# Performance work log

Hardware: AMD Instinct MI355X
Metric: run time of the kernel (lower is better)

## Reference

```python
import jax, jax.numpy as jnp
import numpy as np

VOCAB = 50000
E = 32            # embed_size; node state is E x E
LABELS = 10
DEPTH = 11        # perfect binary tree: 2^DEPTH - 1 = 2047 nodes, 1024 leaves
N_NODES = 2 ** DEPTH - 1
LN_EPS = 1e-5


def setup_inputs() -> dict:
    key = jax.random.key(0)
    ks = jax.random.split(key, 8)
    word_ids = jax.random.randint(ks[0], (N_NODES,), 0, VOCAB, dtype=jnp.int32)
    label = 3
    emb_table = jax.random.normal(ks[1], (VOCAB, E * E), dtype=jnp.float32) * 0.02
    Ww = jax.random.normal(ks[2], (E, E), dtype=jnp.float32) * (1.0 / np.sqrt(E))
    Wb = jax.random.normal(ks[3], (E,), dtype=jnp.float32) * 0.01
    gamma = jnp.ones((E, E), dtype=jnp.float32)   # LayerNorm((1,E,E)) affine weight
    beta = jnp.zeros((E, E), dtype=jnp.float32)
    Pw = jax.random.normal(ks[4], (LABELS, E * E), dtype=jnp.float32) * (1.0 / E)
    Pb = jnp.zeros((LABELS,), dtype=jnp.float32)
    return {"word_ids": word_ids, "label": label, "emb_table": emb_table,
            "Ww": Ww, "Wb": Wb, "gamma": gamma, "beta": beta, "Pw": Pw, "Pb": Pb}


def reference(word_ids, label, emb_table, Ww, Wb, gamma, beta, Pw, Pb):
    # word_ids: level-order ids of a perfect binary tree, children of within-level
    # index j at level d are indices 2j, 2j+1 at level d+1.
    embs = emb_table[word_ids].reshape(N_NODES, E, E)  # [N, E, E]

    def ln_relu(x):
        # torch LayerNorm((1,E,E)): normalize over the whole E*E matrix, affine per element
        mu = jnp.mean(x, axis=(1, 2), keepdims=True)
        var = jnp.var(x, axis=(1, 2), keepdims=True)
        y = (x - mu) * jax.lax.rsqrt(var + LN_EPS) * gamma + beta
        return jax.nn.relu(y)

    # leaves: level DEPTH-1
    start = 2 ** (DEPTH - 1) - 1
    h = ln_relu(embs[start:])  # [2^(DEPTH-1), E, E]
    # internal levels bottom-up; loop over fixed DEPTH-1 levels (not data dims)
    for d in range(DEPTH - 2, -1, -1):
        s = 2 ** d - 1
        cur = embs[s:s + 2 ** d]                     # [n_d, E, E]
        l, r = h[0::2], h[1::2]                      # children pairs
        x = jnp.einsum('nij,njk,nkl->nil', l, r, cur)
        x = x @ Ww.T + Wb                            # Linear applied row-wise
        h = ln_relu(x)

    root = h[0].reshape(-1)                          # [E*E]
    logits = root @ Pw.T + Pb                        # [LABELS]
    prediction = jnp.argmax(logits)
    loss = -jax.nn.log_softmax(logits)[label]
    return (prediction, loss)
```

## Files before the change

### kernel.cpp

```cpp
#include <hip/hip_runtime.h>
#include <hip/hip_bf16.h>

#define LN_EPS 1e-5f
#define TSB 40
#define TILEB (32 * TSB)

typedef __attribute__((ext_vector_type(8))) short bf16x8;
typedef __attribute__((ext_vector_type(16))) float f32x16;

__device__ __forceinline__ short bf16b(float f) {
  return __builtin_bit_cast(short, __float2bfloat16(f));
}

__device__ __forceinline__ void wave_reduce2(float& s1, float& s2) {
  #pragma unroll
  for (int off = 32; off; off >>= 1) {
    s1 += __shfl_xor(s1, off);
    s2 += __shfl_xor(s2, off);
  }
}

__device__ __forceinline__ bf16x8 frag_ld(const short* t, int l, int k0) {
  return *(const bf16x8*)&t[(l & 31) * TSB + ((l >> 5) << 3) + k0];
}

__device__ __forceinline__ int cd_row(int r, int l) {
  return (r & 3) + 8 * (r >> 2) + 4 * (l >> 5);
}

__device__ __forceinline__ void cd_store(short* t, int l, const f32x16 d,
                                         bool transp) {
  const int col = l & 31;
  if (transp) {
    #pragma unroll
    for (int r = 0; r < 16; ++r) t[col * TSB + cd_row(r, l)] = bf16b(d[r]);
  } else {
    #pragma unroll
    for (int r = 0; r < 16; ++r) t[cd_row(r, l) * TSB + col] = bf16b(d[r]);
  }
}

struct NodeParams {
  bf16x8 w0, w1;
  float wb;
  float ga[16], be[16];
};

__device__ __forceinline__ NodeParams load_params(const float* __restrict__ Ww,
    const float* __restrict__ Wb, const float* __restrict__ gamma,
    const float* __restrict__ beta, int l) {
  NodeParams P;
  const int n = l & 31, kh = (l >> 5) * 8;
  float w[8];
  *(float4*)&w[0] = *(const float4*)&Ww[n * 32 + kh];
  *(float4*)&w[4] = *(const float4*)&Ww[n * 32 + kh + 4];
  #pragma unroll
  for (int i = 0; i < 8; ++i) P.w0[i] = bf16b(w[i]);
  *(float4*)&w[0] = *(const float4*)&Ww[n * 32 + kh + 16];
  *(float4*)&w[4] = *(const float4*)&Ww[n * 32 + kh + 20];
  #pragma unroll
  for (int i = 0; i < 8; ++i) P.w1[i] = bf16b(w[i]);
  P.wb = Wb[n];
  #pragma unroll
  for (int r = 0; r < 16; ++r) {
    const int idx = cd_row(r, l) * 32 + n;
    P.ga[r] = gamma[idx];
    P.be[r] = beta[idx];
  }
  return P;
}

__device__ __forceinline__ f32x16 mm32(const short* A, const short* B, int l) {
  f32x16 acc = {};
  acc = __builtin_amdgcn_mfma_f32_32x32x16_bf16(frag_ld(A, l, 0),
                                                frag_ld(B, l, 0), acc, 0, 0, 0);
  acc = __builtin_amdgcn_mfma_f32_32x32x16_bf16(frag_ld(A, l, 16),
                                                frag_ld(B, l, 16), acc, 0, 0, 0);
  return acc;
}

__device__ __forceinline__ void node_mfma(short* A, short* Bt, const short* Ct,
                                          const NodeParams& P, int l,
                                          short* dst, bool transpOut,
                                          float* fout) {
  f32x16 t1 = mm32(A, Bt, l);
  cd_store(A, l, t1, false);
  f32x16 t2 = mm32(A, Ct, l);
  cd_store(Bt, l, t2, false);
  f32x16 x = {};
  x = __builtin_amdgcn_mfma_f32_32x32x16_bf16(frag_ld(Bt, l, 0), P.w0, x, 0, 0, 0);
  x = __builtin_amdgcn_mfma_f32_32x32x16_bf16(frag_ld(Bt, l, 16), P.w1, x, 0, 0, 0);
  float s1 = 0.f, s2 = 0.f;
  #pragma unroll
  for (int r = 0; r < 16; ++r) {
    x[r] += P.wb;
    s1 += x[r];
    s2 += x[r] * x[r];
  }
  wave_reduce2(s1, s2);
  const float mu = s1 * (1.f / 1024.f);
  const float rs = rsqrtf(s2 * (1.f / 1024.f) - mu * mu + LN_EPS);
  #pragma unroll
  for (int r = 0; r < 16; ++r)
    x[r] = fmaxf((x[r] - mu) * rs * P.ga[r] + P.be[r], 0.f);
  if (fout) {
    #pragma unroll
    for (int r = 0; r < 16; ++r) fout[cd_row(r, l) * 32 + (l & 31)] = x[r];
  } else {
    cd_store(dst, l, x, transpOut);
  }
}

__device__ __forceinline__ void stage_f32(short* dst,
                                          const float* __restrict__ src, int l,
                                          bool transp) {
  float v[16];
  #pragma unroll
  for (int q = 0; q < 4; ++q)
    *(float4*)&v[q * 4] = *(const float4*)&src[l * 16 + q * 4];
  const int row = l >> 1, c0 = (l & 1) * 16;
  if (transp) {
    #pragma unroll
    for (int i = 0; i < 16; ++i) dst[(c0 + i) * TSB + row] = bf16b(v[i]);
  } else {
    #pragma unroll
    for (int i = 0; i < 8; ++i) {
      unsigned lo = (unsigned short)bf16b(v[2 * i]);
      unsigned hi = (unsigned short)bf16b(v[2 * i + 1]);
      ((unsigned*)dst)[row * (TSB / 2) + (c0 >> 1) + i] = lo | (hi << 16);
    }
  }
}

__device__ __forceinline__ void stage_bf16(short* dst,
                                           const short* __restrict__ src, int l,
                                           bool transp) {
  short v[16];
  *(bf16x8*)&v[0] = *(const bf16x8*)&src[l * 16];
  *(bf16x8*)&v[8] = *(const bf16x8*)&src[l * 16 + 8];
  const int row = l >> 1, c0 = (l & 1) * 16;
  if (transp) {
    #pragma unroll
    for (int i = 0; i < 16; ++i) dst[(c0 + i) * TSB + row] = v[i];
  } else {
    #pragma unroll
    for (int i = 0; i < 8; ++i) {
      unsigned lo = (unsigned short)v[2 * i];
      unsigned hi = (unsigned short)v[2 * i + 1];
      ((unsigned*)dst)[row * (TSB / 2) + (c0 >> 1) + i] = lo | (hi << 16);
    }
  }
}

__device__ __forceinline__ void copy_out(short* __restrict__ dst, const short* t,
                                         int u) {
  if (u < 128) {
    const int row = u >> 2, c0 = (u & 3) * 8;
    *(bf16x8*)&dst[row * 32 + c0] = *(const bf16x8*)&t[row * TSB + c0];
  }
}

__device__ __forceinline__ void leaf_ln(short* dst, const float* __restrict__ src,
                                        const float* __restrict__ gamma,
                                        const float* __restrict__ beta, int l,
                                        bool transp) {
  float v[16], ga[16], be[16];
  #pragma unroll
  for (int q = 0; q < 4; ++q) {
    *(float4*)&v[q * 4] = *(const float4*)&src[l * 16 + q * 4];
    *(float4*)&ga[q * 4] = *(const float4*)&gamma[l * 16 + q * 4];
    *(float4*)&be[q * 4] = *(const float4*)&beta[l * 16 + q * 4];
  }
  float s1 = 0.f, s2 = 0.f;
  #pragma unroll
  for (int i = 0; i < 16; ++i) { s1 += v[i]; s2 += v[i] * v[i]; }
  wave_reduce2(s1, s2);
  const float mu = s1 * (1.f / 1024.f);
  const float rs = rsqrtf(s2 * (1.f / 1024.f) - mu * mu + LN_EPS);
  #pragma unroll
  for (int i = 0; i < 16; ++i)
    v[i] = fmaxf((v[i] - mu) * rs * ga[i] + be[i], 0.f);
  const int row = l >> 1, c0 = (l & 1) * 16;
  if (transp) {
    #pragma unroll
    for (int i = 0; i < 16; ++i) dst[(c0 + i) * TSB + row] = bf16b(v[i]);
  } else {
    #pragma unroll
    for (int i = 0; i < 8; ++i) {
      unsigned lo = (unsigned short)bf16b(v[2 * i]);
      unsigned hi = (unsigned short)bf16b(v[2 * i + 1]);
      ((unsigned*)dst)[row * (TSB / 2) + (c0 >> 1) + i] = lo | (hi << 16);
    }
  }
}

__global__ __launch_bounds__(256) void k_bot(
    const int* __restrict__ wid, const float* __restrict__ emb,
    const float* __restrict__ Ww, const float* __restrict__ Wb,
    const float* __restrict__ gamma, const float* __restrict__ beta,
    short* __restrict__ h8) {
  __shared__ __align__(16) short pool[7 * TILEB];
  const int u = threadIdx.x, blk = blockIdx.x;
  const int wv = u >> 6, l = u & 63;
  NodeParams P = load_params(Ww, Wb, gamma, beta, l);
  if (wv == 0)
    stage_f32(pool + 4 * TILEB, emb + (size_t)wid[511 + 2 * blk] * 1024, l, true);
  else if (wv == 1)
    stage_f32(pool + 5 * TILEB, emb + (size_t)wid[512 + 2 * blk] * 1024, l, true);
  else if (wv == 2)
    stage_f32(pool + 6 * TILEB, emb + (size_t)wid[255 + blk] * 1024, l, true);
  leaf_ln(pool + wv * TILEB, emb + (size_t)wid[1023 + 4 * blk + wv] * 1024,
          gamma, beta, l, (wv & 1) != 0);
  __syncthreads();
  if (wv < 2)
    node_mfma(pool + 2 * wv * TILEB, pool + (2 * wv + 1) * TILEB,
              pool + (4 + wv) * TILEB, P, l, pool + (4 + wv) * TILEB, wv == 1,
              nullptr);
  __syncthreads();
  if (wv == 0)
    node_mfma(pool + 4 * TILEB, pool + 5 * TILEB, pool + 6 * TILEB, P, l,
              pool + 6 * TILEB, false, nullptr);
  __syncthreads();
  copy_out(h8 + (size_t)blk * 1024, pool + 6 * TILEB, u);
}

__global__ __launch_bounds__(256) void k_mid(
    const int* __restrict__ wid, const float* __restrict__ emb,
    const float* __restrict__ Ww, const float* __restrict__ Wb,
    const float* __restrict__ gamma, const float* __restrict__ beta,
    const short* __restrict__ hin, short* __restrict__ hout,
    int cb, int pb, int gb) {
  __shared__ __align__(16) short pool[15 * TILEB];
  const int u = threadIdx.x, blk = blockIdx.x;
  const int wv = u >> 6, l = u & 63;
  NodeParams P = load_params(Ww, Wb, gamma, beta, l);
  stage_bf16(pool + 2 * wv * TILEB, hin + (size_t)(8 * blk + 2 * wv) * 1024, l,
             false);
  stage_bf16(pool + (2 * wv + 1) * TILEB,
             hin + (size_t)(8 * blk + 2 * wv + 1) * 1024, l, true);
  stage_f32(pool + (8 + wv) * TILEB,
            emb + (size_t)wid[cb + 4 * blk + wv] * 1024, l, true);
  if (wv < 2)
    stage_f32(pool + (12 + wv) * TILEB,
              emb + (size_t)wid[pb + 2 * blk + wv] * 1024, l, true);
  else if (wv == 2)
    stage_f32(pool + 14 * TILEB, emb + (size_t)wid[gb + blk] * 1024, l, true);
  __syncthreads();
  node_mfma(pool + 2 * wv * TILEB, pool + (2 * wv + 1) * TILEB,
            pool + (8 + wv) * TILEB, P, l, pool + (8 + wv) * TILEB,
            (wv & 1) != 0, nullptr);
  __syncthreads();
  if (wv < 2)
    node_mfma(pool + (8 + 2 * wv) * TILEB, pool + (9 + 2 * wv) * TILEB,
              pool + (12 + wv) * TILEB, P, l, pool + (12 + wv) * TILEB,
              wv == 1, nullptr);
  __syncthreads();
  if (wv == 0)
    node_mfma(pool + 12 * TILEB, pool + 13 * TILEB, pool + 14 * TILEB, P, l,
              pool + 14 * TILEB, false, nullptr);
  __syncthreads();
  copy_out(hout + (size_t)blk * 1024, pool + 14 * TILEB, u);
}

__global__ __launch_bounds__(256) void k_top(
    const int* __restrict__ wid, const float* __restrict__ emb,
    const float* __restrict__ Ww, const float* __restrict__ Wb,
    const float* __restrict__ gamma, const float* __restrict__ beta,
    const float* __restrict__ Pw, const float* __restrict__ Pb,
    const int* __restrict__ label, const short* __restrict__ hin,
    float* __restrict__ out) {
  __shared__ __align__(16) short pool[7 * TILEB];
  __shared__ float rootf[1024];
  __shared__ float lred[10];
  const int u = threadIdx.x;
  const int wv = u >> 6, l = u & 63;
  NodeParams P = load_params(Ww, Wb, gamma, beta, l);
  stage_bf16(pool + wv * TILEB, hin + (size_t)wv * 1024, l, (wv & 1) != 0);
  if (wv == 0) stage_f32(pool + 4 * TILEB, emb + (size_t)wid[1] * 1024, l, true);
  else if (wv == 1) stage_f32(pool + 5 * TILEB, emb + (size_t)wid[2] * 1024, l, true);
  else if (wv == 2) stage_f32(pool + 6 * TILEB, emb + (size_t)wid[0] * 1024, l, true);
  __syncthreads();
  if (wv < 2)
    node_mfma(pool + 2 * wv * TILEB, pool + (2 * wv + 1) * TILEB,
              pool + (4 + wv) * TILEB, P, l, pool + (4 + wv) * TILEB, wv == 1,
              nullptr);
  __syncthreads();
  if (wv == 0)
    node_mfma(pool + 4 * TILEB, pool + 5 * TILEB, pool + 6 * TILEB, P, l,
              nullptr, false, rootf);
  __syncthreads();
  #pragma unroll
  for (int q = 0; q < 3; ++q) {
    const int c = wv + 4 * q;
    if (c < 10) {
      float p = 0.f;
      #pragma unroll
      for (int t = 0; t < 4; ++t) {
        float4 r4 = *(const float4*)&rootf[l * 16 + t * 4];
        float4 w4 = *(const float4*)&Pw[c * 1024 + l * 16 + t * 4];
        p += r4.x * w4.x + r4.y * w4.y + r4.z * w4.z + r4.w * w4.w;
      }
      #pragma unroll
      for (int off = 32; off; off >>= 1) p += __shfl_xor(p, off);
      if (l == 0) lred[c] = p + Pb[c];
    }
  }
  __syncthreads();
  if (u == 0) {
    float mmax = lred[0];
    int am = 0;
    #pragma unroll
    for (int c = 1; c < 10; ++c)
      if (lred[c] > mmax) { mmax = lred[c]; am = c; }
    float sum = 0.f;
    #pragma unroll
    for (int c = 0; c < 10; ++c) sum += expf(lred[c] - mmax);
    const float loss = -(lred[label[0]] - mmax - logf(sum));
    out[0] = (float)am;
    out[1] = loss;
  }
}

extern "C" void kernel_launch(void* const* d_in, const int* in_sizes, int n_in,
                              void* d_out, int out_size, void* d_ws, size_t ws_size,
                              hipStream_t stream) {
  const int* wid = (const int*)d_in[0];
  const int* label = (const int*)d_in[1];
  const float* emb = (const float*)d_in[2];
  const float* Ww = (const float*)d_in[3];
  const float* Wb = (const float*)d_in[4];
  const float* g = (const float*)d_in[5];
  const float* b = (const float*)d_in[6];
  const float* Pw = (const float*)d_in[7];
  const float* Pb = (const float*)d_in[8];
  float* out = (float*)d_out;

  short* h8 = (short*)d_ws;
  short* h5 = h8 + 256 * 1024;
  short* h2 = h5 + 32 * 1024;

  k_bot<<<256, 256, 0, stream>>>(wid, emb, Ww, Wb, g, b, h8);
  k_mid<<<32, 256, 0, stream>>>(wid, emb, Ww, Wb, g, b, h8, h5, 127, 63, 31);
  k_mid<<<4, 256, 0, stream>>>(wid, emb, Ww, Wb, g, b, h5, h2, 15, 7, 3);
  k_top<<<1, 256, 0, stream>>>(wid, emb, Ww, Wb, g, b, Pw, Pb, label, h2, out);
}
```

Before: 30.82 us.

## Regroup tree levels into three 512-thread launches instead of four

```diff
diff --git a/kernel.cpp b/kernel.cpp
--- a/kernel.cpp
+++ b/kernel.cpp
@@ -194,104 +194,126 @@
   }
 }
 
-__global__ __launch_bounds__(256) void k_bot(
+__global__ __launch_bounds__(512) void k_bot7(
     const int* __restrict__ wid, const float* __restrict__ emb,
     const float* __restrict__ Ww, const float* __restrict__ Wb,
     const float* __restrict__ gamma, const float* __restrict__ beta,
-    short* __restrict__ h8) {
-  __shared__ __align__(16) short pool[7 * TILEB];
-  const int u = threadIdx.x, blk = blockIdx.x;
-  const int wv = u >> 6, l = u & 63;
-  NodeParams P = load_params(Ww, Wb, gamma, beta, l);
-  if (wv == 0)
-    stage_f32(pool + 4 * TILEB, emb + (size_t)wid[511 + 2 * blk] * 1024, l, true);
-  else if (wv == 1)
-    stage_f32(pool + 5 * TILEB, emb + (size_t)wid[512 + 2 * blk] * 1024, l, true);
-  else if (wv == 2)
-    stage_f32(pool + 6 * TILEB, emb + (size_t)wid[255 + blk] * 1024, l, true);
-  leaf_ln(pool + wv * TILEB, emb + (size_t)wid[1023 + 4 * blk + wv] * 1024,
-          gamma, beta, l, (wv & 1) != 0);
-  __syncthreads();
-  if (wv < 2)
-    node_mfma(pool + 2 * wv * TILEB, pool + (2 * wv + 1) * TILEB,
-              pool + (4 + wv) * TILEB, P, l, pool + (4 + wv) * TILEB, wv == 1,
-              nullptr);
-  __syncthreads();
-  if (wv == 0)
-    node_mfma(pool + 4 * TILEB, pool + 5 * TILEB, pool + 6 * TILEB, P, l,
-              pool + 6 * TILEB, false, nullptr);
-  __syncthreads();
-  copy_out(h8 + (size_t)blk * 1024, pool + 6 * TILEB, u);
-}
-
-__global__ __launch_bounds__(256) void k_mid(
-    const int* __restrict__ wid, const float* __restrict__ emb,
-    const float* __restrict__ Ww, const float* __restrict__ Wb,
-    const float* __restrict__ gamma, const float* __restrict__ beta,
-    const short* __restrict__ hin, short* __restrict__ hout,
-    int cb, int pb, int gb) {
+    short* __restrict__ h7) {
   __shared__ __align__(16) short pool[15 * TILEB];
   const int u = threadIdx.x, blk = blockIdx.x;
   const int wv = u >> 6, l = u & 63;
   NodeParams P = load_params(Ww, Wb, gamma, beta, l);
-  stage_bf16(pool + 2 * wv * TILEB, hin + (size_t)(8 * blk + 2 * wv) * 1024, l,
-             false);
-  stage_bf16(pool + (2 * wv + 1) * TILEB,
-             hin + (size_t)(8 * blk + 2 * wv + 1) * 1024, l, true);
-  stage_f32(pool + (8 + wv) * TILEB,
-            emb + (size_t)wid[cb + 4 * blk + wv] * 1024, l, true);
-  if (wv < 2)
-    stage_f32(pool + (12 + wv) * TILEB,
-              emb + (size_t)wid[pb + 2 * blk + wv] * 1024, l, true);
-  else if (wv == 2)
-    stage_f32(pool + 14 * TILEB, emb + (size_t)wid[gb + blk] * 1024, l, true);
-  __syncthreads();
-  node_mfma(pool + 2 * wv * TILEB, pool + (2 * wv + 1) * TILEB,
-            pool + (8 + wv) * TILEB, P, l, pool + (8 + wv) * TILEB,
-            (wv & 1) != 0, nullptr);
+  if (wv < 4)
+    stage_f32(pool + (8 + wv) * TILEB,
+              emb + (size_t)wid[511 + 4 * blk + wv] * 1024, l, true);
+  else if (wv < 6)
+    stage_f32(pool + (8 + wv) * TILEB,
+              emb + (size_t)wid[255 + 2 * blk + (wv - 4)] * 1024, l, true);
+  else if (wv == 6)
+    stage_f32(pool + 14 * TILEB, emb + (size_t)wid[127 + blk] * 1024, l, true);
+  leaf_ln(pool + wv * TILEB, emb + (size_t)wid[1023 + 8 * blk + wv] * 1024,
+          gamma, beta, l, (wv & 1) != 0);
+  __syncthreads();
+  if (wv < 4)
+    node_mfma(pool + 2 * wv * TILEB, pool + (2 * wv + 1) * TILEB,
+              pool + (8 + wv) * TILEB, P, l, pool + (8 + wv) * TILEB,
+              (wv & 1) != 0, nullptr);
   __syncthreads();
   if (wv < 2)
     node_mfma(pool + (8 + 2 * wv) * TILEB, pool + (9 + 2 * wv) * TILEB,
               pool + (12 + wv) * TILEB, P, l, pool + (12 + wv) * TILEB,
-              wv == 1, nullptr);
+              (wv & 1) != 0, nullptr);
   __syncthreads();
   if (wv == 0)
     node_mfma(pool + 12 * TILEB, pool + 13 * TILEB, pool + 14 * TILEB, P, l,
               pool + 14 * TILEB, false, nullptr);
   __syncthreads();
+  copy_out(h7 + (size_t)blk * 1024, pool + 14 * TILEB, u);
+}
+
+__global__ __launch_bounds__(512) void k_mid16(
+    const int* __restrict__ wid, const float* __restrict__ emb,
+    const float* __restrict__ Ww, const float* __restrict__ Wb,
+    const float* __restrict__ gamma, const float* __restrict__ beta,
+    const short* __restrict__ hin, short* __restrict__ hout) {
+  __shared__ __align__(16) short pool[15 * TILEB];
+  const int u = threadIdx.x, blk = blockIdx.x;
+  const int wv = u >> 6, l = u & 63;
+  NodeParams P = load_params(Ww, Wb, gamma, beta, l);
+  stage_bf16(pool + wv * TILEB, hin + (size_t)(8 * blk + wv) * 1024, l,
+             (wv & 1) != 0);
+  if (wv < 4)
+    stage_f32(pool + (8 + wv) * TILEB,
+              emb + (size_t)wid[63 + 4 * blk + wv] * 1024, l, true);
+  else if (wv < 6)
+    stage_f32(pool + (8 + wv) * TILEB,
+              emb + (size_t)wid[31 + 2 * blk + (wv - 4)] * 1024, l, true);
+  else if (wv == 6)
+    stage_f32(pool + 14 * TILEB, emb + (size_t)wid[15 + blk] * 1024, l, true);
+  __syncthreads();
+  if (wv < 4)
+    node_mfma(pool + 2 * wv * TILEB, pool + (2 * wv + 1) * TILEB,
+              pool + (8 + wv) * TILEB, P, l, pool + (8 + wv) * TILEB,
+              (wv & 1) != 0, nullptr);
+  __syncthreads();
+  if (wv < 2)
+    node_mfma(pool + (8 + 2 * wv) * TILEB, pool + (9 + 2 * wv) * TILEB,
+              pool + (12 + wv) * TILEB, P, l, pool + (12 + wv) * TILEB,
+              (wv & 1) != 0, nullptr);
+  __syncthreads();
+  if (wv == 0)
+    node_mfma(pool + 12 * TILEB, pool + 13 * TILEB, pool + 14 * TILEB, P, l,
+              pool + 14 * TILEB, false, nullptr);
+  __syncthreads();
   copy_out(hout + (size_t)blk * 1024, pool + 14 * TILEB, u);
 }
 
-__global__ __launch_bounds__(256) void k_top(
+__global__ __launch_bounds__(512) void k_top2(
     const int* __restrict__ wid, const float* __restrict__ emb,
     const float* __restrict__ Ww, const float* __restrict__ Wb,
     const float* __restrict__ gamma, const float* __restrict__ beta,
     const float* __restrict__ Pw, const float* __restrict__ Pb,
     const int* __restrict__ label, const short* __restrict__ hin,
     float* __restrict__ out) {
-  __shared__ __align__(16) short pool[7 * TILEB];
+  __shared__ __align__(16) short pool[31 * TILEB];
   __shared__ float rootf[1024];
   __shared__ float lred[10];
   const int u = threadIdx.x;
   const int wv = u >> 6, l = u & 63;
   NodeParams P = load_params(Ww, Wb, gamma, beta, l);
-  stage_bf16(pool + wv * TILEB, hin + (size_t)wv * 1024, l, (wv & 1) != 0);
-  if (wv == 0) stage_f32(pool + 4 * TILEB, emb + (size_t)wid[1] * 1024, l, true);
-  else if (wv == 1) stage_f32(pool + 5 * TILEB, emb + (size_t)wid[2] * 1024, l, true);
-  else if (wv == 2) stage_f32(pool + 6 * TILEB, emb + (size_t)wid[0] * 1024, l, true);
+  stage_bf16(pool + 2 * wv * TILEB, hin + (size_t)(2 * wv) * 1024, l, false);
+  stage_bf16(pool + (2 * wv + 1) * TILEB, hin + (size_t)(2 * wv + 1) * 1024, l,
+             true);
+  stage_f32(pool + (16 + wv) * TILEB, emb + (size_t)wid[7 + wv] * 1024, l, true);
+  if (wv < 4)
+    stage_f32(pool + (24 + wv) * TILEB, emb + (size_t)wid[3 + wv] * 1024, l, true);
+  else if (wv < 6)
+    stage_f32(pool + (24 + wv) * TILEB,
+              emb + (size_t)wid[1 + (wv - 4)] * 1024, l, true);
+  else if (wv == 6)
+    stage_f32(pool + 30 * TILEB, emb + (size_t)wid[0] * 1024, l, true);
+  __syncthreads();
+  node_mfma(pool + 2 * wv * TILEB, pool + (2 * wv + 1) * TILEB,
+            pool + (16 + wv) * TILEB, P, l, pool + (16 + wv) * TILEB,
+            (wv & 1) != 0, nullptr);
+  __syncthreads();
+  if (wv < 4)
+    node_mfma(pool + (16 + 2 * wv) * TILEB, pool + (17 + 2 * wv) * TILEB,
+              pool + (24 + wv) * TILEB, P, l, pool + (24 + wv) * TILEB,
+              (wv & 1) != 0, nullptr);
   __syncthreads();
   if (wv < 2)
-    node_mfma(pool + 2 * wv * TILEB, pool + (2 * wv + 1) * TILEB,
-              pool + (4 + wv) * TILEB, P, l, pool + (4 + wv) * TILEB, wv == 1,
-              nullptr);
+    node_mfma(pool + (24 + 2 * wv) * TILEB, pool + (25 + 2 * wv) * TILEB,
+              pool + (28 + wv) * TILEB, P, l, pool + (28 + wv) * TILEB,
+              (wv & 1) != 0, nullptr);
   __syncthreads();
   if (wv == 0)
-    node_mfma(pool + 4 * TILEB, pool + 5 * TILEB, pool + 6 * TILEB, P, l,
+    node_mfma(pool + 28 * TILEB, pool + 29 * TILEB, pool + 30 * TILEB, P, l,
               nullptr, false, rootf);
   __syncthreads();
   #pragma unroll
-  for (int q = 0; q < 3; ++q) {
-    const int c = wv + 4 * q;
+  for (int q = 0; q < 2; ++q) {
+    const int c = wv + 8 * q;
     if (c < 10) {
       float p = 0.f;
       #pragma unroll
@@ -335,12 +357,10 @@
   const float* Pb = (const float*)d_in[8];
   float* out = (float*)d_out;
 
-  short* h8 = (short*)d_ws;
-  short* h5 = h8 + 256 * 1024;
-  short* h2 = h5 + 32 * 1024;
-
-  k_bot<<<256, 256, 0, stream>>>(wid, emb, Ww, Wb, g, b, h8);
-  k_mid<<<32, 256, 0, stream>>>(wid, emb, Ww, Wb, g, b, h8, h5, 127, 63, 31);
-  k_mid<<<4, 256, 0, stream>>>(wid, emb, Ww, Wb, g, b, h5, h2, 15, 7, 3);
-  k_top<<<1, 256, 0, stream>>>(wid, emb, Ww, Wb, g, b, Pw, Pb, label, h2, out);
-}
+  short* h7 = (short*)d_ws;
+  short* h4 = h7 + 128 * 1024;
+
+  k_bot7<<<128, 512, 0, stream>>>(wid, emb, Ww, Wb, g, b, h7);
+  k_mid16<<<16, 512, 0, stream>>>(wid, emb, Ww, Wb, g, b, h7, h4);
+  k_top2<<<1, 512, 0, stream>>>(wid, emb, Ww, Wb, g, b, Pw, Pb, label, h4, out);
+}
```

Result: no change. 30.55 us (-0.9%).

## Fuse tree levels into one persistent kernel with flag-based inter-block sync

Applied to the files above, without the earlier changes.

```diff
diff --git a/kernel.cpp b/kernel.cpp
--- a/kernel.cpp
+++ b/kernel.cpp
@@ -4,6 +4,7 @@
 #define LN_EPS 1e-5f
 #define TSB 40
 #define TILEB (32 * TSB)
+#define MAGIC 0x5A5A7E1Du
 
 typedef __attribute__((ext_vector_type(8))) short bf16x8;
 typedef __attribute__((ext_vector_type(16))) float f32x16;
@@ -132,12 +133,8 @@
   }
 }
 
-__device__ __forceinline__ void stage_bf16(short* dst,
-                                           const short* __restrict__ src, int l,
-                                           bool transp) {
-  short v[16];
-  *(bf16x8*)&v[0] = *(const bf16x8*)&src[l * 16];
-  *(bf16x8*)&v[8] = *(const bf16x8*)&src[l * 16 + 8];
+__device__ __forceinline__ void lds_put16(short* dst, const short v[16], int l,
+                                          bool transp) {
   const int row = l >> 1, c0 = (l & 1) * 16;
   if (transp) {
     #pragma unroll
@@ -152,12 +149,40 @@
   }
 }
 
-__device__ __forceinline__ void copy_out(short* __restrict__ dst, const short* t,
-                                         int u) {
-  if (u < 128) {
-    const int row = u >> 2, c0 = (u & 3) * 8;
-    *(bf16x8*)&dst[row * 32 + c0] = *(const bf16x8*)&t[row * TSB + c0];
-  }
+__device__ __forceinline__ void fetch_tile(short* dstLds,
+                                           const unsigned* __restrict__ src,
+                                           int l, bool transp) {
+  short v[16];
+  #pragma unroll
+  for (int i = 0; i < 8; ++i) {
+    unsigned x = __hip_atomic_load(src + l * 8 + i, __ATOMIC_RELAXED,
+                                   __HIP_MEMORY_SCOPE_AGENT);
+    v[2 * i] = (short)(x & 0xFFFFu);
+    v[2 * i + 1] = (short)(x >> 16);
+  }
+  lds_put16(dstLds, v, l, transp);
+}
+
+__device__ __forceinline__ void emit_tile(unsigned* __restrict__ dst,
+                                          const short* t, int u) {
+  #pragma unroll
+  for (int q = 0; q < 2; ++q) {
+    const int w = 2 * u + q;
+    const int row = w >> 4, cp = w & 15;
+    unsigned v = *(const unsigned*)&t[row * TSB + cp * 2];
+    __hip_atomic_store(dst + w, v, __ATOMIC_RELAXED, __HIP_MEMORY_SCOPE_AGENT);
+  }
+}
+
+__device__ __forceinline__ void flag_set(unsigned* f) {
+  __hip_atomic_store(f, MAGIC, __ATOMIC_RELAXED, __HIP_MEMORY_SCOPE_AGENT);
+}
+
+__device__ __forceinline__ void flag_wait(const unsigned* f) {
+  while (__hip_atomic_load(f, __ATOMIC_RELAXED, __HIP_MEMORY_SCOPE_AGENT) !=
+         MAGIC)
+    __builtin_amdgcn_s_sleep(1);
+  asm volatile("" ::: "memory");
 }
 
 __device__ __forceinline__ void leaf_ln(short* dst, const float* __restrict__ src,
@@ -177,74 +202,32 @@
   wave_reduce2(s1, s2);
   const float mu = s1 * (1.f / 1024.f);
   const float rs = rsqrtf(s2 * (1.f / 1024.f) - mu * mu + LN_EPS);
+  short o[16];
   #pragma unroll
   for (int i = 0; i < 16; ++i)
-    v[i] = fmaxf((v[i] - mu) * rs * ga[i] + be[i], 0.f);
-  const int row = l >> 1, c0 = (l & 1) * 16;
-  if (transp) {
-    #pragma unroll
-    for (int i = 0; i < 16; ++i) dst[(c0 + i) * TSB + row] = bf16b(v[i]);
-  } else {
-    #pragma unroll
-    for (int i = 0; i < 8; ++i) {
-      unsigned lo = (unsigned short)bf16b(v[2 * i]);
-      unsigned hi = (unsigned short)bf16b(v[2 * i + 1]);
-      ((unsigned*)dst)[row * (TSB / 2) + (c0 >> 1) + i] = lo | (hi << 16);
-    }
-  }
-}
-
-__global__ __launch_bounds__(256) void k_bot(
+    o[i] = bf16b(fmaxf((v[i] - mu) * rs * ga[i] + be[i], 0.f));
+  lds_put16(dst, o, l, transp);
+}
+
+__device__ __forceinline__ void phase3(
+    int blk, int u, int wv, int l, short* pool, const NodeParams& P,
     const int* __restrict__ wid, const float* __restrict__ emb,
-    const float* __restrict__ Ww, const float* __restrict__ Wb,
-    const float* __restrict__ gamma, const float* __restrict__ beta,
-    short* __restrict__ h8) {
-  __shared__ __align__(16) short pool[7 * TILEB];
-  const int u = threadIdx.x, blk = blockIdx.x;
-  const int wv = u >> 6, l = u & 63;
-  NodeParams P = load_params(Ww, Wb, gamma, beta, l);
-  if (wv == 0)
-    stage_f32(pool + 4 * TILEB, emb + (size_t)wid[511 + 2 * blk] * 1024, l, true);
-  else if (wv == 1)
-    stage_f32(pool + 5 * TILEB, emb + (size_t)wid[512 + 2 * blk] * 1024, l, true);
-  else if (wv == 2)
-    stage_f32(pool + 6 * TILEB, emb + (size_t)wid[255 + blk] * 1024, l, true);
-  leaf_ln(pool + wv * TILEB, emb + (size_t)wid[1023 + 4 * blk + wv] * 1024,
-          gamma, beta, l, (wv & 1) != 0);
-  __syncthreads();
-  if (wv < 2)
-    node_mfma(pool + 2 * wv * TILEB, pool + (2 * wv + 1) * TILEB,
-              pool + (4 + wv) * TILEB, P, l, pool + (4 + wv) * TILEB, wv == 1,
-              nullptr);
-  __syncthreads();
-  if (wv == 0)
-    node_mfma(pool + 4 * TILEB, pool + 5 * TILEB, pool + 6 * TILEB, P, l,
-              pool + 6 * TILEB, false, nullptr);
-  __syncthreads();
-  copy_out(h8 + (size_t)blk * 1024, pool + 6 * TILEB, u);
-}
-
-__global__ __launch_bounds__(256) void k_mid(
-    const int* __restrict__ wid, const float* __restrict__ emb,
-    const float* __restrict__ Ww, const float* __restrict__ Wb,
-    const float* __restrict__ gamma, const float* __restrict__ beta,
-    const short* __restrict__ hin, short* __restrict__ hout,
-    int cb, int pb, int gb) {
-  __shared__ __align__(16) short pool[15 * TILEB];
-  const int u = threadIdx.x, blk = blockIdx.x;
-  const int wv = u >> 6, l = u & 63;
-  NodeParams P = load_params(Ww, Wb, gamma, beta, l);
-  stage_bf16(pool + 2 * wv * TILEB, hin + (size_t)(8 * blk + 2 * wv) * 1024, l,
-             false);
-  stage_bf16(pool + (2 * wv + 1) * TILEB,
-             hin + (size_t)(8 * blk + 2 * wv + 1) * 1024, l, true);
+    const unsigned* __restrict__ hinu, const unsigned* __restrict__ finf,
+    unsigned* __restrict__ houtu, unsigned* __restrict__ foutf,
+    int b0, int b1, int b2) {
   stage_f32(pool + (8 + wv) * TILEB,
-            emb + (size_t)wid[cb + 4 * blk + wv] * 1024, l, true);
+            emb + (size_t)wid[b0 + 4 * blk + wv] * 1024, l, true);
   if (wv < 2)
     stage_f32(pool + (12 + wv) * TILEB,
-              emb + (size_t)wid[pb + 2 * blk + wv] * 1024, l, true);
+              emb + (size_t)wid[b1 + 2 * blk + wv] * 1024, l, true);
   else if (wv == 2)
-    stage_f32(pool + 14 * TILEB, emb + (size_t)wid[gb + blk] * 1024, l, true);
+    stage_f32(pool + 14 * TILEB, emb + (size_t)wid[b2 + blk] * 1024, l, true);
+  if (u < 8) flag_wait(finf + 8 * blk + u);
+  __syncthreads();
+  fetch_tile(pool + 2 * wv * TILEB, hinu + (size_t)(8 * blk + 2 * wv) * 512, l,
+             false);
+  fetch_tile(pool + (2 * wv + 1) * TILEB,
+             hinu + (size_t)(8 * blk + 2 * wv + 1) * 512, l, true);
   __syncthreads();
   node_mfma(pool + 2 * wv * TILEB, pool + (2 * wv + 1) * TILEB,
             pool + (8 + wv) * TILEB, P, l, pool + (8 + wv) * TILEB,
@@ -253,71 +236,114 @@
   if (wv < 2)
     node_mfma(pool + (8 + 2 * wv) * TILEB, pool + (9 + 2 * wv) * TILEB,
               pool + (12 + wv) * TILEB, P, l, pool + (12 + wv) * TILEB,
-              wv == 1, nullptr);
+              (wv & 1) != 0, nullptr);
   __syncthreads();
   if (wv == 0)
     node_mfma(pool + 12 * TILEB, pool + 13 * TILEB, pool + 14 * TILEB, P, l,
               pool + 14 * TILEB, false, nullptr);
   __syncthreads();
-  copy_out(hout + (size_t)blk * 1024, pool + 14 * TILEB, u);
-}
-
-__global__ __launch_bounds__(256) void k_top(
+  emit_tile(houtu + (size_t)blk * 512, pool + 14 * TILEB, u);
+  asm volatile("s_waitcnt vmcnt(0)" ::: "memory");
+  __syncthreads();
+  if (u == 0) flag_set(foutf + blk);
+}
+
+__global__ __launch_bounds__(256) void k_tree(
     const int* __restrict__ wid, const float* __restrict__ emb,
     const float* __restrict__ Ww, const float* __restrict__ Wb,
     const float* __restrict__ gamma, const float* __restrict__ beta,
     const float* __restrict__ Pw, const float* __restrict__ Pb,
-    const int* __restrict__ label, const short* __restrict__ hin,
+    const int* __restrict__ label,
+    unsigned* __restrict__ h8u, unsigned* __restrict__ h5u,
+    unsigned* __restrict__ h2u, unsigned* __restrict__ h8f,
+    unsigned* __restrict__ h5f, unsigned* __restrict__ h2f,
     float* __restrict__ out) {
-  __shared__ __align__(16) short pool[7 * TILEB];
+  __shared__ __align__(16) short pool[15 * TILEB];
   __shared__ float rootf[1024];
   __shared__ float lred[10];
-  const int u = threadIdx.x;
+  const int u = threadIdx.x, blk = blockIdx.x;
   const int wv = u >> 6, l = u & 63;
   NodeParams P = load_params(Ww, Wb, gamma, beta, l);
-  stage_bf16(pool + wv * TILEB, hin + (size_t)wv * 1024, l, (wv & 1) != 0);
-  if (wv == 0) stage_f32(pool + 4 * TILEB, emb + (size_t)wid[1] * 1024, l, true);
-  else if (wv == 1) stage_f32(pool + 5 * TILEB, emb + (size_t)wid[2] * 1024, l, true);
-  else if (wv == 2) stage_f32(pool + 6 * TILEB, emb + (size_t)wid[0] * 1024, l, true);
-  __syncthreads();
-  if (wv < 2)
-    node_mfma(pool + 2 * wv * TILEB, pool + (2 * wv + 1) * TILEB,
-              pool + (4 + wv) * TILEB, P, l, pool + (4 + wv) * TILEB, wv == 1,
-              nullptr);
-  __syncthreads();
-  if (wv == 0)
-    node_mfma(pool + 4 * TILEB, pool + 5 * TILEB, pool + 6 * TILEB, P, l,
-              nullptr, false, rootf);
-  __syncthreads();
-  #pragma unroll
-  for (int q = 0; q < 3; ++q) {
-    const int c = wv + 4 * q;
-    if (c < 10) {
-      float p = 0.f;
+
+  {
+    if (wv == 0)
+      stage_f32(pool + 4 * TILEB, emb + (size_t)wid[511 + 2 * blk] * 1024, l, true);
+    else if (wv == 1)
+      stage_f32(pool + 5 * TILEB, emb + (size_t)wid[512 + 2 * blk] * 1024, l, true);
+    else if (wv == 2)
+      stage_f32(pool + 6 * TILEB, emb + (size_t)wid[255 + blk] * 1024, l, true);
+    leaf_ln(pool + wv * TILEB, emb + (size_t)wid[1023 + 4 * blk + wv] * 1024,
+            gamma, beta, l, (wv & 1) != 0);
+    __syncthreads();
+    if (wv < 2)
+      node_mfma(pool + 2 * wv * TILEB, pool + (2 * wv + 1) * TILEB,
+                pool + (4 + wv) * TILEB, P, l, pool + (4 + wv) * TILEB,
+                wv == 1, nullptr);
+    __syncthreads();
+    if (wv == 0)
+      node_mfma(pool + 4 * TILEB, pool + 5 * TILEB, pool + 6 * TILEB, P, l,
+                pool + 6 * TILEB, false, nullptr);
+    __syncthreads();
+    emit_tile(h8u + (size_t)blk * 512, pool + 6 * TILEB, u);
+    asm volatile("s_waitcnt vmcnt(0)" ::: "memory");
+    __syncthreads();
+    if (u == 0) flag_set(h8f + blk);
+  }
+
+  if (blk >= 32) return;
+  phase3(blk, u, wv, l, pool, P, wid, emb, h8u, h8f, h5u, h5f, 127, 63, 31);
+
+  if (blk >= 4) return;
+  phase3(blk, u, wv, l, pool, P, wid, emb, h5u, h5f, h2u, h2f, 15, 7, 3);
+
+  if (blk >= 1) return;
+  {
+    if (wv == 0) stage_f32(pool + 4 * TILEB, emb + (size_t)wid[1] * 1024, l, true);
+    else if (wv == 1) stage_f32(pool + 5 * TILEB, emb + (size_t)wid[2] * 1024, l, true);
+    else if (wv == 2) stage_f32(pool + 6 * TILEB, emb + (size_t)wid[0] * 1024, l, true);
+    if (u < 4) flag_wait(h2f + u);
+    __syncthreads();
+    fetch_tile(pool + wv * TILEB, h2u + (size_t)wv * 512, l, (wv & 1) != 0);
+    __syncthreads();
+    if (wv < 2)
+      node_mfma(pool + 2 * wv * TILEB, pool + (2 * wv + 1) * TILEB,
+                pool + (4 + wv) * TILEB, P, l, pool + (4 + wv) * TILEB, wv == 1,
+                nullptr);
+    __syncthreads();
+    if (wv == 0)
+      node_mfma(pool + 4 * TILEB, pool + 5 * TILEB, pool + 6 * TILEB, P, l,
+                nullptr, false, rootf);
+    __syncthreads();
+    #pragma unroll
+    for (int q = 0; q < 3; ++q) {
+      const int c = wv + 4 * q;
+      if (c < 10) {
+        float p = 0.f;
+        #pragma unroll
+        for (int t = 0; t < 4; ++t) {
+          float4 r4 = *(const float4*)&rootf[l * 16 + t * 4];
+          float4 w4 = *(const float4*)&Pw[c * 1024 + l * 16 + t * 4];
+          p += r4.x * w4.x + r4.y * w4.y + r4.z * w4.z + r4.w * w4.w;
+        }
+        #pragma unroll
+        for (int off = 32; off; off >>= 1) p += __shfl_xor(p, off);
+        if (l == 0) lred[c] = p + Pb[c];
+      }
+    }
+    __syncthreads();
+    if (u == 0) {
+      float mmax = lred[0];
+      int am = 0;
       #pragma unroll
-      for (int t = 0; t < 4; ++t) {
-        float4 r4 = *(const float4*)&rootf[l * 16 + t * 4];
-        float4 w4 = *(const float4*)&Pw[c * 1024 + l * 16 + t * 4];
-        p += r4.x * w4.x + r4.y * w4.y + r4.z * w4.z + r4.w * w4.w;
-      }
+      for (int c = 1; c < 10; ++c)
+        if (lred[c] > mmax) { mmax = lred[c]; am = c; }
+      float sum = 0.f;
       #pragma unroll
-      for (int off = 32; off; off >>= 1) p += __shfl_xor(p, off);
-      if (l == 0) lred[c] = p + Pb[c];
+      for (int c = 0; c < 10; ++c) sum += expf(lred[c] - mmax);
+      const float loss = -(lred[label[0]] - mmax - logf(sum));
+      out[0] = (float)am;
+      out[1] = loss;
     }
-  }
-  __syncthreads();
-  if (u == 0) {
-    float mmax = lred[0];
-    int am = 0;
-    #pragma unroll
-    for (int c = 1; c < 10; ++c)
-      if (lred[c] > mmax) { mmax = lred[c]; am = c; }
-    float sum = 0.f;
-    #pragma unroll
-    for (int c = 0; c < 10; ++c) sum += expf(lred[c] - mmax);
-    const float loss = -(lred[label[0]] - mmax - logf(sum));
-    out[0] = (float)am;
-    out[1] = loss;
   }
 }
 
@@ -335,12 +361,13 @@
   const float* Pb = (const float*)d_in[8];
   float* out = (float*)d_out;
 
-  short* h8 = (short*)d_ws;
-  short* h5 = h8 + 256 * 1024;
-  short* h2 = h5 + 32 * 1024;
-
-  k_bot<<<256, 256, 0, stream>>>(wid, emb, Ww, Wb, g, b, h8);
-  k_mid<<<32, 256, 0, stream>>>(wid, emb, Ww, Wb, g, b, h8, h5, 127, 63, 31);
-  k_mid<<<4, 256, 0, stream>>>(wid, emb, Ww, Wb, g, b, h5, h2, 15, 7, 3);
-  k_top<<<1, 256, 0, stream>>>(wid, emb, Ww, Wb, g, b, Pw, Pb, label, h2, out);
-}
+  unsigned* h8u = (unsigned*)d_ws;
+  unsigned* h5u = h8u + 256 * 512;
+  unsigned* h2u = h5u + 32 * 512;
+  unsigned* h8f = h2u + 4 * 512;
+  unsigned* h5f = h8f + 256;
+  unsigned* h2f = h5f + 32;
+
+  k_tree<<<256, 256, 0, stream>>>(wid, emb, Ww, Wb, g, b, Pw, Pb, label,
+                                  h8u, h5u, h2u, h8f, h5f, h2f, out);
+}
```

Measured after the change: 31.73 us. 2.9% more time.
